# Performance work log

Measured on AMD Instinct MI355X. Metric: run time of the kernel, lower is better.

## Reference

```python
import jax, jax.numpy as jnp
import numpy as np

N_NODES = 50000
N_EDGES = 800000
DIM_IN = 64
DIM_H = 32
HEADS = 4
NUM_CLASSES = 10
NEG_SLOPE = 0.2  # DGL GATv2Conv default negative_slope


def _gatv2_layer(x, W_src, b_src, W_dst, b_dst, attn, src, dst):
    """DGL GATv2Conv (share_weights=False, eval mode so feat_drop is identity).
    x: [N, F_in]; attn: [H, D]; returns [N, H, D]."""
    N = x.shape[0]
    H, D = attn.shape
    fs = (x @ W_src + b_src).reshape(N, H, D)  # source projection
    fd = (x @ W_dst + b_dst).reshape(N, H, D)  # destination projection
    # per-edge additive attention: leaky_relu(fs[u] + fd[v]) . attn  -> [E, H]
    e = jax.nn.leaky_relu(fs[src] + fd[dst], NEG_SLOPE)  # [E, H, D]
    s = jnp.einsum('ehd,hd->eh', e, attn)  # [E, H]
    # edge softmax over incoming edges of each destination node
    smax = jax.lax.stop_gradient(
        jax.ops.segment_max(s, dst, num_segments=N))  # [N, H]
    es = jnp.exp(s - smax[dst])
    denom = jax.ops.segment_sum(es, dst, num_segments=N)  # [N, H]
    alpha = es / denom[dst]
    # weighted scatter-aggregate of source features
    out = jax.ops.segment_sum(alpha[:, :, None] * fs[src], dst, num_segments=N)
    return out  # [N, H, D]


def setup_inputs() -> dict:
    key = jax.random.key(0)
    ks = jax.random.split(key, 16)
    sc = 0.05
    inp = {
        'g_feats': jax.random.normal(ks[0], (N_NODES, DIM_IN), jnp.float32),
        'edge_src': jax.random.randint(ks[1], (N_EDGES,), 0, N_NODES, jnp.int32),
        'edge_dst': jax.random.randint(ks[2], (N_EDGES,), 0, N_NODES, jnp.int32),
        # input embedding Linear(dim_in, dim_h)
        'W_in': jax.random.normal(ks[3], (DIM_IN, DIM_H), jnp.float32) * sc,
        'b_in': jnp.zeros((DIM_H,), jnp.float32),
        # GATv2 layer 1: Linear(dim_h, heads*dim_h) for src/dst + attn [H, D]
        'W1_src': jax.random.normal(ks[4], (DIM_H, HEADS * DIM_H), jnp.float32) * sc,
        'b1_src': jnp.zeros((HEADS * DIM_H,), jnp.float32),
        'W1_dst': jax.random.normal(ks[5], (DIM_H, HEADS * DIM_H), jnp.float32) * sc,
        'b1_dst': jnp.zeros((HEADS * DIM_H,), jnp.float32),
        'attn1': jax.random.normal(ks[6], (HEADS, DIM_H), jnp.float32) * sc,
        # GATv2 layer 2
        'W2_src': jax.random.normal(ks[7], (DIM_H, HEADS * DIM_H), jnp.float32) * sc,
        'b2_src': jnp.zeros((HEADS * DIM_H,), jnp.float32),
        'W2_dst': jax.random.normal(ks[8], (DIM_H, HEADS * DIM_H), jnp.float32) * sc,
        'b2_dst': jnp.zeros((HEADS * DIM_H,), jnp.float32),
        'attn2': jax.random.normal(ks[9], (HEADS, DIM_H), jnp.float32) * sc,
        # MLP head: Linear(dim_h, dim_h) -> relu -> (dropout: eval) -> Linear(dim_h, num_classes)
        'Wh1': jax.random.normal(ks[10], (DIM_H, DIM_H), jnp.float32) * sc,
        'bh1': jnp.zeros((DIM_H,), jnp.float32),
        'Wh2': jax.random.normal(ks[11], (DIM_H, NUM_CLASSES), jnp.float32) * sc,
        'bh2': jnp.zeros((NUM_CLASSES,), jnp.float32),
    }
    return inp


def reference(g_feats, W_in, b_in,
              W1_src, b1_src, W1_dst, b1_dst, attn1,
              W2_src, b2_src, W2_dst, b2_dst, attn2,
              Wh1, bh1, Wh2, bh2,
              edge_src, edge_dst):
    x = g_feats @ W_in + b_in  # input embedding, [N, dim_h]
    h = _gatv2_layer(x, W1_src, b1_src, W1_dst, b1_dst, attn1, edge_src, edge_dst)
    h = jax.nn.relu(h.mean(axis=1))  # mean over heads -> [N, dim_h]
    h = _gatv2_layer(h, W2_src, b2_src, W2_dst, b2_dst, attn2, edge_src, edge_dst)
    h = h.mean(axis=1)  # [N, dim_h]
    # dgl.readout_nodes(op='mean') over the single graph -> [1, dim_h]
    g = h.mean(axis=0, keepdims=True)
    g = jax.nn.relu(g @ Wh1 + bh1)  # head (dropout inactive in eval)
    logits = g @ Wh2 + bh2
    return jax.nn.softmax(logits, axis=-1)  # [1, num_classes]
```

## Files before the change

kernel.cpp:

```cpp
#include <hip/hip_runtime.h>
#include <hip/hip_bf16.h>

#define N_NODES 50000
#define N_EDGES 800000
#define DIM_IN 64
#define DIM_H 32
#define HEADS 4
#define NCLS 10
#define NEG 0.2f
#define NBUCK 196


__global__ void k_bhist(const int* __restrict__ dst, int* __restrict__ bh) {
    __shared__ int lh[NBUCK];
    for (int i = threadIdx.x; i < NBUCK; i += 256) lh[i] = 0;
    __syncthreads();
    int base = blockIdx.x * 1024 + threadIdx.x;
#pragma unroll
    for (int r = 0; r < 4; r++) {
        int e = base + r * 256;
        if (e < N_EDGES) atomicAdd(&lh[dst[e] >> 8], 1);
    }
    __syncthreads();
    for (int i = threadIdx.x; i < NBUCK; i += 256) {
        int c = lh[i];
        if (c) atomicAdd(&bh[i], c);
    }
}

__global__ void k_bscan(const int* __restrict__ bh, int* __restrict__ bbase,
                        int* __restrict__ gcur) {
    __shared__ int s[256];
    int t = threadIdx.x;
    int v = (t < NBUCK) ? bh[t] : 0;
    s[t] = v;
    __syncthreads();
    for (int off = 1; off < 256; off <<= 1) {
        int u = (t >= off) ? s[t - off] : 0;
        __syncthreads();
        s[t] += u;
        __syncthreads();
    }
    int excl = s[t] - v;
    if (t < NBUCK) {
        bbase[t] = excl;
        gcur[t] = excl;
    }
    if (t == 0) bbase[NBUCK] = N_EDGES;
}

__global__ void k_bin(const int* __restrict__ src, const int* __restrict__ dst,
                      int* __restrict__ gcur, unsigned* __restrict__ stage) {
    __shared__ int lh[NBUCK], chunk[NBUCK];
    int t = threadIdx.x;
    for (int i = t; i < NBUCK; i += 256) lh[i] = 0;
    __syncthreads();
    int e0 = blockIdx.x * 4096;
    unsigned pk[16];
    int bk[16];
#pragma unroll
    for (int r = 0; r < 16; r++) {
        int e = e0 + r * 256 + t;
        bool ok = e < N_EDGES;
        int s = ok ? src[e] : 0;
        int d = ok ? dst[e] : 0;
        bk[r] = ok ? (d >> 8) : -1;
        pk[r] = (unsigned)s | ((unsigned)(d & 255) << 16);
        if (ok) atomicAdd(&lh[bk[r]], 1);
    }
    __syncthreads();
    for (int i = t; i < NBUCK; i += 256) {
        int c = lh[i];
        chunk[i] = c ? atomicAdd(&gcur[i], c) : 0;
        lh[i] = 0;
    }
    __syncthreads();
#pragma unroll
    for (int r = 0; r < 16; r++) {
        if (bk[r] >= 0) {
            int lp = atomicAdd(&lh[bk[r]], 1);
            stage[chunk[bk[r]] + lp] = pk[r];
        }
    }
}

__global__ void k_csr(const unsigned* __restrict__ stage, const int* __restrict__ bbase,
                      int* __restrict__ row, int* __restrict__ adj) {
    __shared__ int lcnt[256], lcur[256], sc[256];
    int b = blockIdx.x, t = threadIdx.x;
    int s0 = bbase[b], s1 = bbase[b + 1];
    lcnt[t] = 0;
    __syncthreads();
    for (int i = s0 + t; i < s1; i += 256) atomicAdd(&lcnt[stage[i] >> 16], 1);
    __syncthreads();
    int v = lcnt[t];
    sc[t] = v;
    __syncthreads();
    for (int off = 1; off < 256; off <<= 1) {
        int u = (t >= off) ? sc[t - off] : 0;
        __syncthreads();
        sc[t] += u;
        __syncthreads();
    }
    int excl = sc[t] - v;
    int n = b * 256 + t;
    if (n < N_NODES) row[n] = s0 + excl;
    if (b == NBUCK - 1 && t == 0) row[N_NODES] = N_EDGES;
    lcur[t] = s0 + excl;
    __syncthreads();
    for (int i = s0 + t; i < s1; i += 256) {
        unsigned p = stage[i];
        int pos = atomicAdd(&lcur[p >> 16], 1);
        adj[pos] = (int)(p & 0xFFFFu);
    }
}


__device__ __forceinline__ unsigned short f2bf(float v) {
    unsigned u = __builtin_bit_cast(unsigned, v);
    u += 0x7FFFu + ((u >> 16) & 1u);
    return (unsigned short)(u >> 16);
}
__device__ __forceinline__ float bf2f(unsigned short h) {
    return __builtin_bit_cast(float, (unsigned)h << 16);
}

__global__ __launch_bounds__(256, 1) void k_fused1(
    const float* __restrict__ gf, const float* __restrict__ W_in,
    const float* __restrict__ b_in, const float* __restrict__ W1s,
    const float* __restrict__ b1s, const float* __restrict__ W1d,
    const float* __restrict__ b1d, unsigned short* __restrict__ fsh,
    float* __restrict__ fd) {
    __shared__ float4 xb[4][2][8];
    int lane = threadIdx.x & 63;
    int wvl = threadIdx.x >> 6;
    int wave = (blockIdx.x * 256 + threadIdx.x) >> 6;
    int c = lane & 31, h = lane >> 5;
    int n0 = wave * 16;
    if (n0 >= N_NODES) return;
    float wi[32];
#pragma unroll
    for (int k = 0; k < 32; k++) wi[k] = W_in[(h * 32 + k) * DIM_H + c];
    float bc = b_in[c];
    const float4* Wb = (lane < 32) ? (const float4*)W1s : (const float4*)W1d;
    const float4* bb = (lane < 32) ? (const float4*)b1s : (const float4*)b1d;
    float4 w[32];
#pragma unroll
    for (int k = 0; k < 32; k++) w[k] = Wb[k * 32 + c];
    float4 bias = bb[c];
#pragma unroll 2
    for (int i = 0; i < 16; i++) {
        int nu = __builtin_amdgcn_readfirstlane(n0 + i);
        const float4* gr = (const float4*)(gf + (size_t)nu * DIM_IN + h * 32);
        float a1 = 0.f;
#pragma unroll
        for (int k4 = 0; k4 < 8; k4++) {
            float4 xv = gr[k4];
            a1 += xv.x * wi[k4 * 4 + 0];
            a1 += xv.y * wi[k4 * 4 + 1];
            a1 += xv.z * wi[k4 * 4 + 2];
            a1 += xv.w * wi[k4 * 4 + 3];
        }
        a1 += __shfl_xor(a1, 32, 64);
        if (lane < 32) ((float*)&xb[wvl][i & 1][0])[c] = a1 + bc;
        float4 acc = bias;
#pragma unroll
        for (int k4 = 0; k4 < 8; k4++) {
            float4 xv = xb[wvl][i & 1][k4];
#pragma unroll
            for (int j = 0; j < 4; j++) {
                float xk = (j == 0) ? xv.x : (j == 1) ? xv.y : (j == 2) ? xv.z : xv.w;
                float4 wk = w[k4 * 4 + j];
                acc.x += xk * wk.x;
                acc.y += xk * wk.y;
                acc.z += xk * wk.z;
                acc.w += xk * wk.w;
            }
        }
        if (lane < 32) {
            ushort4 o;
            o.x = f2bf(acc.x);
            o.y = f2bf(acc.y);
            o.z = f2bf(acc.z);
            o.w = f2bf(acc.w);
            *(ushort4*)&fsh[(size_t)nu * 128 + c * 4] = o;
        } else {
            *(float4*)&fd[(size_t)nu * 128 + c * 4] = acc;
        }
    }
}

__global__ __launch_bounds__(256, 1) void k_proj(
    const float* __restrict__ x, const float* __restrict__ Wsrc,
    const float* __restrict__ bsrc, const float* __restrict__ Wdst,
    const float* __restrict__ bdst, unsigned short* __restrict__ fsh,
    float* __restrict__ fd) {
    int lane = threadIdx.x & 63;
    int wave = (blockIdx.x * 256 + threadIdx.x) >> 6;
    int cl = lane & 31;
    int n0 = wave * 16;
    if (n0 >= N_NODES) return;
    const float4* Wb = (lane < 32) ? (const float4*)Wsrc : (const float4*)Wdst;
    const float4* bb = (lane < 32) ? (const float4*)bsrc : (const float4*)bdst;
    float4 w[32];
#pragma unroll
    for (int k = 0; k < 32; k++) w[k] = Wb[k * 32 + cl];
    float4 bias = bb[cl];
#pragma unroll 2
    for (int i = 0; i < 16; i++) {
        int nu = __builtin_amdgcn_readfirstlane(n0 + i);
        const float4* xr = (const float4*)(x + (size_t)nu * DIM_H);
        float4 acc = bias;
#pragma unroll
        for (int k4 = 0; k4 < 8; k4++) {
            float4 xv = xr[k4];
#pragma unroll
            for (int j = 0; j < 4; j++) {
                float xk = (j == 0) ? xv.x : (j == 1) ? xv.y : (j == 2) ? xv.z : xv.w;
                float4 wk = w[k4 * 4 + j];
                acc.x += xk * wk.x;
                acc.y += xk * wk.y;
                acc.z += xk * wk.z;
                acc.w += xk * wk.w;
            }
        }
        if (lane < 32) {
            ushort4 o;
            o.x = f2bf(acc.x);
            o.y = f2bf(acc.y);
            o.z = f2bf(acc.z);
            o.w = f2bf(acc.w);
            *(ushort4*)&fsh[(size_t)nu * 128 + cl * 4] = o;
        } else {
            *(float4*)&fd[(size_t)nu * 128 + cl * 4] = acc;
        }
    }
}

__device__ __forceinline__ void pair_acc(const unsigned short* fsh, unsigned byteoff,
                                         float4 fdv, float4 a4, float4& acc,
                                         float& den, bool valid) {
    ushort4 u = *(const ushort4*)((const char*)fsh + byteoff);
    float f0 = bf2f(u.x), f1 = bf2f(u.y), f2 = bf2f(u.z), f3 = bf2f(u.w);
    float t0 = f0 + fdv.x; t0 = fmaxf(t0, NEG * t0);
    float t1 = f1 + fdv.y; t1 = fmaxf(t1, NEG * t1);
    float t2 = f2 + fdv.z; t2 = fmaxf(t2, NEG * t2);
    float t3 = f3 + fdv.w; t3 = fmaxf(t3, NEG * t3);
    float p = t0 * a4.x + t1 * a4.y + t2 * a4.z + t3 * a4.w;
    p += __shfl_xor(p, 1, 64);
    p += __shfl_xor(p, 2, 64);
    p += __shfl_xor(p, 4, 64);
    float w = __expf(p);
    if (!valid) w = 0.f;
    den += w;
    acc.x += w * f0;
    acc.y += w * f1;
    acc.z += w * f2;
    acc.w += w * f3;
}

__global__ void k_gather(const unsigned short* __restrict__ fsh,
                         const float* __restrict__ fd, const float* __restrict__ attn,
                         const int* __restrict__ row, const int* __restrict__ adj,
                         float* __restrict__ xout, int do_relu) {
    int wave = threadIdx.x >> 6;
    int lane = threadIdx.x & 63;
    int n = blockIdx.x * 4 + wave;
    if (n >= N_NODES) return;
    int sub = lane & 31, e2 = lane >> 5;
    unsigned suboff = (unsigned)sub << 3;
    float4 a4 = ((const float4*)attn)[sub];
    float4 fdv = ((const float4*)(fd + (size_t)n * 128))[sub];
    float4 acc = {0.f, 0.f, 0.f, 0.f};
    float den = 0.f;
    int beg = row[n], end = row[n + 1];
    for (int base = beg; base < end; base += 64) {
        int m = end - base;
        if (m > 64) m = 64;
        int myadj = (lane < m) ? adj[base + lane] : 0;
        int j = 0;
        for (; j + 8 <= m; j += 8) {
            unsigned o0 = ((unsigned)__shfl(myadj, j + 0 + e2, 64) << 8) + suboff;
            unsigned o1 = ((unsigned)__shfl(myadj, j + 2 + e2, 64) << 8) + suboff;
            unsigned o2 = ((unsigned)__shfl(myadj, j + 4 + e2, 64) << 8) + suboff;
            unsigned o3 = ((unsigned)__shfl(myadj, j + 6 + e2, 64) << 8) + suboff;
            pair_acc(fsh, o0, fdv, a4, acc, den, true);
            pair_acc(fsh, o1, fdv, a4, acc, den, true);
            pair_acc(fsh, o2, fdv, a4, acc, den, true);
            pair_acc(fsh, o3, fdv, a4, acc, den, true);
        }
        for (; j < m; j += 2) {
            int idx = j + e2;
            bool valid = idx < m;
            unsigned o = ((unsigned)__shfl(myadj, valid ? idx : j, 64) << 8) + suboff;
            pair_acc(fsh, o, fdv, a4, acc, den, valid);
        }
    }
    den += __shfl_xor(den, 32, 64);
    acc.x += __shfl_xor(acc.x, 32, 64);
    acc.y += __shfl_xor(acc.y, 32, 64);
    acc.z += __shfl_xor(acc.z, 32, 64);
    acc.w += __shfl_xor(acc.w, 32, 64);
    float inv = den > 0.f ? 0.25f / den : 0.f;
    float4 o;
    o.x = acc.x * inv;
    o.y = acc.y * inv;
    o.z = acc.z * inv;
    o.w = acc.w * inv;
    o.x += __shfl_xor(o.x, 8, 64);
    o.y += __shfl_xor(o.y, 8, 64);
    o.z += __shfl_xor(o.z, 8, 64);
    o.w += __shfl_xor(o.w, 8, 64);
    o.x += __shfl_xor(o.x, 16, 64);
    o.y += __shfl_xor(o.y, 16, 64);
    o.z += __shfl_xor(o.z, 16, 64);
    o.w += __shfl_xor(o.w, 16, 64);
    if (do_relu) {
        o.x = o.x > 0.f ? o.x : 0.f;
        o.y = o.y > 0.f ? o.y : 0.f;
        o.z = o.z > 0.f ? o.z : 0.f;
        o.w = o.w > 0.f ? o.w : 0.f;
    }
    if (lane < 8) ((float4*)(xout + (size_t)n * 32))[lane] = o;
}

__global__ void k_reduce(const float* __restrict__ x, float* __restrict__ partial) {
    int d = threadIdx.x & 31, g = threadIdx.x >> 5;
    float acc = 0.f;
    int stride = gridDim.x * 8;
    for (int n = blockIdx.x * 8 + g; n < N_NODES; n += stride) {
        acc += x[(size_t)n * 32 + d];
    }
    __shared__ float s[256];
    s[threadIdx.x] = acc;
    __syncthreads();
    for (int off = 128; off >= 32; off >>= 1) {
        if (threadIdx.x < off) s[threadIdx.x] += s[threadIdx.x + off];
        __syncthreads();
    }
    if (threadIdx.x < 32) partial[blockIdx.x * 32 + threadIdx.x] = s[threadIdx.x];
}

__global__ void k_final(const float* __restrict__ partial, const float* __restrict__ Wh1,
                        const float* __restrict__ bh1, const float* __restrict__ Wh2,
                        const float* __restrict__ bh2, float* __restrict__ out) {
    __shared__ float gv[32], gh[32], lg[16];
    int t = threadIdx.x;
    if (t < 32) {
        float s = 0.f;
        for (int b = 0; b < 256; b++) s += partial[b * 32 + t];
        gv[t] = s * (1.f / (float)N_NODES);
    }
    __syncthreads();
    if (t < 32) {
        float s = bh1[t];
        for (int d = 0; d < 32; d++) s += gv[d] * Wh1[d * 32 + t];
        gh[t] = s > 0.f ? s : 0.f;
    }
    __syncthreads();
    if (t < NCLS) {
        float s = bh2[t];
        for (int j = 0; j < 32; j++) s += gh[j] * Wh2[j * NCLS + t];
        lg[t] = s;
    }
    __syncthreads();
    if (t == 0) {
        float m = lg[0];
        for (int c = 1; c < NCLS; c++) m = fmaxf(m, lg[c]);
        float ex[NCLS], sum = 0.f;
        for (int c = 0; c < NCLS; c++) {
            ex[c] = __expf(lg[c] - m);
            sum += ex[c];
        }
        float inv = 1.f / sum;
        for (int c = 0; c < NCLS; c++) out[c] = ex[c] * inv;
    }
}

extern "C" void kernel_launch(void* const* d_in, const int* in_sizes, int n_in,
                              void* d_out, int out_size, void* d_ws, size_t ws_size,
                              hipStream_t stream) {
    const float* g_feats = (const float*)d_in[0];
    const int* edge_src = (const int*)d_in[1];
    const int* edge_dst = (const int*)d_in[2];
    const float* W_in = (const float*)d_in[3];
    const float* b_in = (const float*)d_in[4];
    const float* W1_src = (const float*)d_in[5];
    const float* b1_src = (const float*)d_in[6];
    const float* W1_dst = (const float*)d_in[7];
    const float* b1_dst = (const float*)d_in[8];
    const float* attn1 = (const float*)d_in[9];
    const float* W2_src = (const float*)d_in[10];
    const float* b2_src = (const float*)d_in[11];
    const float* W2_dst = (const float*)d_in[12];
    const float* b2_dst = (const float*)d_in[13];
    const float* attn2 = (const float*)d_in[14];
    const float* Wh1 = (const float*)d_in[15];
    const float* bh1 = (const float*)d_in[16];
    const float* Wh2 = (const float*)d_in[17];
    const float* bh2 = (const float*)d_in[18];

    float* x = (float*)d_ws;
    unsigned short* fsh = (unsigned short*)(x + (size_t)N_NODES * 32);
    float* fd = (float*)(fsh + (size_t)N_NODES * 128);
    float* partial = fd + (size_t)N_NODES * 128;
    int* row = (int*)(partial + 256 * 32);
    int* bh = row + N_NODES + 1;
    int* bbase = bh + NBUCK;
    int* gcur = bbase + NBUCK + 1;
    unsigned* stage = (unsigned*)(gcur + NBUCK);
    int* adj = (int*)(stage + N_EDGES);

    const int WB = (N_NODES + 63) / 64;

    hipMemsetAsync(bh, 0, NBUCK * sizeof(int), stream);
    k_bhist<<<(N_EDGES + 1023) / 1024, 256, 0, stream>>>(edge_dst, bh);
    k_bscan<<<1, 256, 0, stream>>>(bh, bbase, gcur);
    k_bin<<<(N_EDGES + 4095) / 4096, 256, 0, stream>>>(edge_src, edge_dst, gcur, stage);
    k_csr<<<NBUCK, 256, 0, stream>>>(stage, bbase, row, adj);

    k_fused1<<<WB, 256, 0, stream>>>(g_feats, W_in, b_in, W1_src, b1_src, W1_dst,
                                     b1_dst, fsh, fd);
    k_gather<<<(N_NODES + 3) / 4, 256, 0, stream>>>(fsh, fd, attn1, row, adj, x, 1);

    k_proj<<<WB, 256, 0, stream>>>(x, W2_src, b2_src, W2_dst, b2_dst, fsh, fd);
    k_gather<<<(N_NODES + 3) / 4, 256, 0, stream>>>(fsh, fd, attn2, row, adj, x, 0);

    k_reduce<<<256, 256, 0, stream>>>(x, partial);
    k_final<<<1, 256, 0, stream>>>(partial, Wh1, bh1, Wh2, bh2, (float*)d_out);
}
```

Measured before the change: 226.1 us.

## Store source features as scaled fp8, shrink adjacency, fuse readout into gather

Source projections are now stored as fp8 with a fixed scale factor instead of bf16, which halves the bytes per gathered edge. The attention vector and normalisation are rescaled to compensate. Adjacency indices become 16-bit, the projection kernels process 25 nodes per wave with a different launch bound, and the second gather reduces the node mean directly into partial sums, so the separate reduce kernel is gone. fp8 quantisation risks accuracy loss, and the fused readout adds shared and global atomics.

```diff
diff --git a/kernel.cpp b/kernel.cpp
--- a/kernel.cpp
+++ b/kernel.cpp
@@ -9,6 +9,10 @@
 #define NCLS 10
 #define NEG 0.2f
 #define NBUCK 196
+#define NPW 25
+#define FSCALE 16.0f
+
+typedef float floatx2 __attribute__((ext_vector_type(2)));
 
 
 __global__ void k_bhist(const int* __restrict__ dst, int* __restrict__ bh) {
@@ -85,7 +89,7 @@
 }
 
 __global__ void k_csr(const unsigned* __restrict__ stage, const int* __restrict__ bbase,
-                      int* __restrict__ row, int* __restrict__ adj) {
+                      int* __restrict__ row, unsigned short* __restrict__ adj) {
     __shared__ int lcnt[256], lcur[256], sc[256];
     int b = blockIdx.x, t = threadIdx.x;
     int s0 = bbase[b], s1 = bbase[b + 1];
@@ -111,32 +115,22 @@
     for (int i = s0 + t; i < s1; i += 256) {
         unsigned p = stage[i];
         int pos = atomicAdd(&lcur[p >> 16], 1);
-        adj[pos] = (int)(p & 0xFFFFu);
-    }
-}
-
-
-__device__ __forceinline__ unsigned short f2bf(float v) {
-    unsigned u = __builtin_bit_cast(unsigned, v);
-    u += 0x7FFFu + ((u >> 16) & 1u);
-    return (unsigned short)(u >> 16);
-}
-__device__ __forceinline__ float bf2f(unsigned short h) {
-    return __builtin_bit_cast(float, (unsigned)h << 16);
-}
-
-__global__ __launch_bounds__(256, 1) void k_fused1(
+        adj[pos] = (unsigned short)(p & 0xFFFFu);
+    }
+}
+
+__global__ __launch_bounds__(256, 2) void k_fused1(
     const float* __restrict__ gf, const float* __restrict__ W_in,
     const float* __restrict__ b_in, const float* __restrict__ W1s,
     const float* __restrict__ b1s, const float* __restrict__ W1d,
-    const float* __restrict__ b1d, unsigned short* __restrict__ fsh,
+    const float* __restrict__ b1d, unsigned char* __restrict__ fsh,
     float* __restrict__ fd) {
     __shared__ float4 xb[4][2][8];
     int lane = threadIdx.x & 63;
     int wvl = threadIdx.x >> 6;
     int wave = (blockIdx.x * 256 + threadIdx.x) >> 6;
     int c = lane & 31, h = lane >> 5;
-    int n0 = wave * 16;
+    int n0 = wave * NPW;
     if (n0 >= N_NODES) return;
     float wi[32];
 #pragma unroll
@@ -149,7 +143,7 @@
     for (int k = 0; k < 32; k++) w[k] = Wb[k * 32 + c];
     float4 bias = bb[c];
 #pragma unroll 2
-    for (int i = 0; i < 16; i++) {
+    for (int i = 0; i < NPW; i++) {
         int nu = __builtin_amdgcn_readfirstlane(n0 + i);
         const float4* gr = (const float4*)(gf + (size_t)nu * DIM_IN + h * 32);
         float a1 = 0.f;
@@ -178,27 +172,31 @@
             }
         }
         if (lane < 32) {
-            ushort4 o;
-            o.x = f2bf(acc.x);
-            o.y = f2bf(acc.y);
-            o.z = f2bf(acc.z);
-            o.w = f2bf(acc.w);
-            *(ushort4*)&fsh[(size_t)nu * 128 + c * 4] = o;
+            int pk = __builtin_amdgcn_cvt_pk_fp8_f32(acc.x * FSCALE, acc.y * FSCALE,
+                                                     0, false);
+            pk = __builtin_amdgcn_cvt_pk_fp8_f32(acc.z * FSCALE, acc.w * FSCALE,
+                                                 pk, true);
+            *(int*)&fsh[(size_t)nu * 128 + c * 4] = pk;
         } else {
-            *(float4*)&fd[(size_t)nu * 128 + c * 4] = acc;
-        }
-    }
-}
-
-__global__ __launch_bounds__(256, 1) void k_proj(
+            float4 o;
+            o.x = acc.x * FSCALE;
+            o.y = acc.y * FSCALE;
+            o.z = acc.z * FSCALE;
+            o.w = acc.w * FSCALE;
+            *(float4*)&fd[(size_t)nu * 128 + c * 4] = o;
+        }
+    }
+}
+
+__global__ __launch_bounds__(256, 2) void k_proj(
     const float* __restrict__ x, const float* __restrict__ Wsrc,
     const float* __restrict__ bsrc, const float* __restrict__ Wdst,
-    const float* __restrict__ bdst, unsigned short* __restrict__ fsh,
+    const float* __restrict__ bdst, unsigned char* __restrict__ fsh,
     float* __restrict__ fd) {
     int lane = threadIdx.x & 63;
     int wave = (blockIdx.x * 256 + threadIdx.x) >> 6;
     int cl = lane & 31;
-    int n0 = wave * 16;
+    int n0 = wave * NPW;
     if (n0 >= N_NODES) return;
     const float4* Wb = (lane < 32) ? (const float4*)Wsrc : (const float4*)Wdst;
     const float4* bb = (lane < 32) ? (const float4*)bsrc : (const float4*)bdst;
@@ -207,7 +205,7 @@
     for (int k = 0; k < 32; k++) w[k] = Wb[k * 32 + cl];
     float4 bias = bb[cl];
 #pragma unroll 2
-    for (int i = 0; i < 16; i++) {
+    for (int i = 0; i < NPW; i++) {
         int nu = __builtin_amdgcn_readfirstlane(n0 + i);
         const float4* xr = (const float4*)(x + (size_t)nu * DIM_H);
         float4 acc = bias;
@@ -225,27 +223,31 @@
             }
         }
         if (lane < 32) {
-            ushort4 o;
-            o.x = f2bf(acc.x);
-            o.y = f2bf(acc.y);
-            o.z = f2bf(acc.z);
-            o.w = f2bf(acc.w);
-            *(ushort4*)&fsh[(size_t)nu * 128 + cl * 4] = o;
+            int pk = __builtin_amdgcn_cvt_pk_fp8_f32(acc.x * FSCALE, acc.y * FSCALE,
+                                                     0, false);
+            pk = __builtin_amdgcn_cvt_pk_fp8_f32(acc.z * FSCALE, acc.w * FSCALE,
+                                                 pk, true);
+            *(int*)&fsh[(size_t)nu * 128 + cl * 4] = pk;
         } else {
-            *(float4*)&fd[(size_t)nu * 128 + cl * 4] = acc;
-        }
-    }
-}
-
-__device__ __forceinline__ void pair_acc(const unsigned short* fsh, unsigned byteoff,
-                                         float4 fdv, float4 a4, float4& acc,
-                                         float& den, bool valid) {
-    ushort4 u = *(const ushort4*)((const char*)fsh + byteoff);
-    float f0 = bf2f(u.x), f1 = bf2f(u.y), f2 = bf2f(u.z), f3 = bf2f(u.w);
-    float t0 = f0 + fdv.x; t0 = fmaxf(t0, NEG * t0);
-    float t1 = f1 + fdv.y; t1 = fmaxf(t1, NEG * t1);
-    float t2 = f2 + fdv.z; t2 = fmaxf(t2, NEG * t2);
-    float t3 = f3 + fdv.w; t3 = fmaxf(t3, NEG * t3);
+            float4 o;
+            o.x = acc.x * FSCALE;
+            o.y = acc.y * FSCALE;
+            o.z = acc.z * FSCALE;
+            o.w = acc.w * FSCALE;
+            *(float4*)&fd[(size_t)nu * 128 + cl * 4] = o;
+        }
+    }
+}
+
+__device__ __forceinline__ void pair_acc(unsigned u, const float4& fdv,
+                                         const float4& a4, float4& acc, float& den,
+                                         bool valid) {
+    floatx2 f01 = __builtin_amdgcn_cvt_pk_f32_fp8((int)u, false);
+    floatx2 f23 = __builtin_amdgcn_cvt_pk_f32_fp8((int)u, true);
+    float t0 = f01.x + fdv.x; t0 = fmaxf(t0, NEG * t0);
+    float t1 = f01.y + fdv.y; t1 = fmaxf(t1, NEG * t1);
+    float t2 = f23.x + fdv.z; t2 = fmaxf(t2, NEG * t2);
+    float t3 = f23.y + fdv.w; t3 = fmaxf(t3, NEG * t3);
     float p = t0 * a4.x + t1 * a4.y + t2 * a4.z + t3 * a4.w;
     p += __shfl_xor(p, 1, 64);
     p += __shfl_xor(p, 2, 64);
@@ -253,23 +255,34 @@
     float w = __expf(p);
     if (!valid) w = 0.f;
     den += w;
-    acc.x += w * f0;
-    acc.y += w * f1;
-    acc.z += w * f2;
-    acc.w += w * f3;
-}
-
-__global__ void k_gather(const unsigned short* __restrict__ fsh,
+    acc.x += w * f01.x;
+    acc.y += w * f01.y;
+    acc.z += w * f23.x;
+    acc.w += w * f23.y;
+}
+
+__global__ void k_gather(const unsigned char* __restrict__ fsh,
                          const float* __restrict__ fd, const float* __restrict__ attn,
-                         const int* __restrict__ row, const int* __restrict__ adj,
-                         float* __restrict__ xout, int do_relu) {
-    int wave = threadIdx.x >> 6;
-    int lane = threadIdx.x & 63;
+                         const int* __restrict__ row,
+                         const unsigned short* __restrict__ adj,
+                         float* __restrict__ xout, float* __restrict__ gpart,
+                         int mode) {
+    __shared__ float bsum[32];
+    int tid = threadIdx.x;
+    if (mode) {
+        if (tid < 32) bsum[tid] = 0.f;
+        __syncthreads();
+    }
+    int wave = tid >> 6;
+    int lane = tid & 63;
     int n = blockIdx.x * 4 + wave;
-    if (n >= N_NODES) return;
     int sub = lane & 31, e2 = lane >> 5;
-    unsigned suboff = (unsigned)sub << 3;
+    unsigned suboff = (unsigned)sub << 2;
     float4 a4 = ((const float4*)attn)[sub];
+    a4.x *= (1.f / FSCALE);
+    a4.y *= (1.f / FSCALE);
+    a4.z *= (1.f / FSCALE);
+    a4.w *= (1.f / FSCALE);
     float4 fdv = ((const float4*)(fd + (size_t)n * 128))[sub];
     float4 acc = {0.f, 0.f, 0.f, 0.f};
     float den = 0.f;
@@ -277,23 +290,28 @@
     for (int base = beg; base < end; base += 64) {
         int m = end - base;
         if (m > 64) m = 64;
-        int myadj = (lane < m) ? adj[base + lane] : 0;
+        int myadj = (lane < m) ? (int)adj[base + lane] : 0;
         int j = 0;
         for (; j + 8 <= m; j += 8) {
-            unsigned o0 = ((unsigned)__shfl(myadj, j + 0 + e2, 64) << 8) + suboff;
-            unsigned o1 = ((unsigned)__shfl(myadj, j + 2 + e2, 64) << 8) + suboff;
-            unsigned o2 = ((unsigned)__shfl(myadj, j + 4 + e2, 64) << 8) + suboff;
-            unsigned o3 = ((unsigned)__shfl(myadj, j + 6 + e2, 64) << 8) + suboff;
-            pair_acc(fsh, o0, fdv, a4, acc, den, true);
-            pair_acc(fsh, o1, fdv, a4, acc, den, true);
-            pair_acc(fsh, o2, fdv, a4, acc, den, true);
-            pair_acc(fsh, o3, fdv, a4, acc, den, true);
+            unsigned o0 = ((unsigned)__shfl(myadj, j + 0 + e2, 64) << 7) + suboff;
+            unsigned o1 = ((unsigned)__shfl(myadj, j + 2 + e2, 64) << 7) + suboff;
+            unsigned o2 = ((unsigned)__shfl(myadj, j + 4 + e2, 64) << 7) + suboff;
+            unsigned o3 = ((unsigned)__shfl(myadj, j + 6 + e2, 64) << 7) + suboff;
+            unsigned u0 = *(const unsigned*)(fsh + o0);
+            unsigned u1 = *(const unsigned*)(fsh + o1);
+            unsigned u2 = *(const unsigned*)(fsh + o2);
+            unsigned u3 = *(const unsigned*)(fsh + o3);
+            pair_acc(u0, fdv, a4, acc, den, true);
+            pair_acc(u1, fdv, a4, acc, den, true);
+            pair_acc(u2, fdv, a4, acc, den, true);
+            pair_acc(u3, fdv, a4, acc, den, true);
         }
         for (; j < m; j += 2) {
             int idx = j + e2;
             bool valid = idx < m;
-            unsigned o = ((unsigned)__shfl(myadj, valid ? idx : j, 64) << 8) + suboff;
-            pair_acc(fsh, o, fdv, a4, acc, den, valid);
+            unsigned o = ((unsigned)__shfl(myadj, valid ? idx : j, 64) << 7) + suboff;
+            unsigned u = *(const unsigned*)(fsh + o);
+            pair_acc(u, fdv, a4, acc, den, valid);
         }
     }
     den += __shfl_xor(den, 32, 64);
@@ -301,7 +319,7 @@
     acc.y += __shfl_xor(acc.y, 32, 64);
     acc.z += __shfl_xor(acc.z, 32, 64);
     acc.w += __shfl_xor(acc.w, 32, 64);
-    float inv = den > 0.f ? 0.25f / den : 0.f;
+    float inv = den > 0.f ? (0.25f / FSCALE) / den : 0.f;
     float4 o;
     o.x = acc.x * inv;
     o.y = acc.y * inv;
@@ -315,40 +333,34 @@
     o.y += __shfl_xor(o.y, 16, 64);
     o.z += __shfl_xor(o.z, 16, 64);
     o.w += __shfl_xor(o.w, 16, 64);
-    if (do_relu) {
-        o.x = o.x > 0.f ? o.x : 0.f;
-        o.y = o.y > 0.f ? o.y : 0.f;
-        o.z = o.z > 0.f ? o.z : 0.f;
-        o.w = o.w > 0.f ? o.w : 0.f;
-    }
-    if (lane < 8) ((float4*)(xout + (size_t)n * 32))[lane] = o;
-}
-
-__global__ void k_reduce(const float* __restrict__ x, float* __restrict__ partial) {
-    int d = threadIdx.x & 31, g = threadIdx.x >> 5;
-    float acc = 0.f;
-    int stride = gridDim.x * 8;
-    for (int n = blockIdx.x * 8 + g; n < N_NODES; n += stride) {
-        acc += x[(size_t)n * 32 + d];
-    }
-    __shared__ float s[256];
-    s[threadIdx.x] = acc;
-    __syncthreads();
-    for (int off = 128; off >= 32; off >>= 1) {
-        if (threadIdx.x < off) s[threadIdx.x] += s[threadIdx.x + off];
-        __syncthreads();
-    }
-    if (threadIdx.x < 32) partial[blockIdx.x * 32 + threadIdx.x] = s[threadIdx.x];
-}
-
-__global__ void k_final(const float* __restrict__ partial, const float* __restrict__ Wh1,
+    if (mode == 0) {
+        if (lane < 8) {
+            o.x = fmaxf(o.x, 0.f);
+            o.y = fmaxf(o.y, 0.f);
+            o.z = fmaxf(o.z, 0.f);
+            o.w = fmaxf(o.w, 0.f);
+            ((float4*)(xout + (size_t)n * 32))[lane] = o;
+        }
+    } else {
+        if (lane < 8) {
+            atomicAdd(&bsum[lane * 4 + 0], o.x);
+            atomicAdd(&bsum[lane * 4 + 1], o.y);
+            atomicAdd(&bsum[lane * 4 + 2], o.z);
+            atomicAdd(&bsum[lane * 4 + 3], o.w);
+        }
+        __syncthreads();
+        if (tid < 32) atomicAdd(&gpart[(blockIdx.x & 63) * 32 + tid], bsum[tid]);
+    }
+}
+
+__global__ void k_final(const float* __restrict__ gpart, const float* __restrict__ Wh1,
                         const float* __restrict__ bh1, const float* __restrict__ Wh2,
                         const float* __restrict__ bh2, float* __restrict__ out) {
     __shared__ float gv[32], gh[32], lg[16];
     int t = threadIdx.x;
     if (t < 32) {
         float s = 0.f;
-        for (int b = 0; b < 256; b++) s += partial[b * 32 + t];
+        for (int b = 0; b < 64; b++) s += gpart[b * 32 + t];
         gv[t] = s * (1.f / (float)N_NODES);
     }
     __syncthreads();
@@ -401,19 +413,20 @@
     const float* bh2 = (const float*)d_in[18];
 
     float* x = (float*)d_ws;
-    unsigned short* fsh = (unsigned short*)(x + (size_t)N_NODES * 32);
+    unsigned char* fsh = (unsigned char*)(x + (size_t)N_NODES * 32);
     float* fd = (float*)(fsh + (size_t)N_NODES * 128);
-    float* partial = fd + (size_t)N_NODES * 128;
-    int* row = (int*)(partial + 256 * 32);
-    int* bh = row + N_NODES + 1;
+    float* gpart = fd + (size_t)N_NODES * 128;
+    int* bh = (int*)(gpart + 64 * 32);
     int* bbase = bh + NBUCK;
     int* gcur = bbase + NBUCK + 1;
-    unsigned* stage = (unsigned*)(gcur + NBUCK);
-    int* adj = (int*)(stage + N_EDGES);
-
-    const int WB = (N_NODES + 63) / 64;
-
-    hipMemsetAsync(bh, 0, NBUCK * sizeof(int), stream);
+    int* row = gcur + NBUCK;
+    unsigned* stage = (unsigned*)(row + N_NODES + 1);
+    unsigned short* adj = (unsigned short*)(stage + N_EDGES);
+
+    const int WB = (N_NODES / NPW + 3) / 4;
+
+    hipMemsetAsync(gpart, 0, (64 * 32 + NBUCK) * sizeof(int), stream);
+
     k_bhist<<<(N_EDGES + 1023) / 1024, 256, 0, stream>>>(edge_dst, bh);
     k_bscan<<<1, 256, 0, stream>>>(bh, bbase, gcur);
     k_bin<<<(N_EDGES + 4095) / 4096, 256, 0, stream>>>(edge_src, edge_dst, gcur, stage);
@@ -421,11 +434,10 @@
 
     k_fused1<<<WB, 256, 0, stream>>>(g_feats, W_in, b_in, W1_src, b1_src, W1_dst,
                                      b1_dst, fsh, fd);
-    k_gather<<<(N_NODES + 3) / 4, 256, 0, stream>>>(fsh, fd, attn1, row, adj, x, 1);
+    k_gather<<<N_NODES / 4, 256, 0, stream>>>(fsh, fd, attn1, row, adj, x, gpart, 0);
 
     k_proj<<<WB, 256, 0, stream>>>(x, W2_src, b2_src, W2_dst, b2_dst, fsh, fd);
-    k_gather<<<(N_NODES + 3) / 4, 256, 0, stream>>>(fsh, fd, attn2, row, adj, x, 0);
-
-    k_reduce<<<256, 256, 0, stream>>>(x, partial);
-    k_final<<<1, 256, 0, stream>>>(partial, Wh1, bh1, Wh2, bh2, (float*)d_out);
-}
+    k_gather<<<N_NODES / 4, 256, 0, stream>>>(fsh, fd, attn2, row, adj, x, gpart, 1);
+
+    k_final<<<1, 256, 0, stream>>>(gpart, Wh1, bh1, Wh2, bh2, (float*)d_out);
+}
```

After: 186.4 us. 17.6% less time.
